# Kernel tuning notes

Hardware: AMD Instinct MI355X
Metric: run time of the kernel (lower is better)

The kernel has to match this reference:

```python
import jax, jax.numpy as jnp
import numpy as np
from jax import lax

DN = ('NCDHW', 'OIDHW', 'NCDHW')


def _ln(x, w, b, eps=1e-5):
    m = jnp.mean(x, -1, keepdims=True)
    v = jnp.mean((x - m) ** 2, -1, keepdims=True)
    return (x - m) * lax.rsqrt(v + eps) * w + b


def _gelu(x):
    return jax.nn.gelu(x, approximate=False)


def _dwconv3(v, w, b, groups):
    # depthwise 3x3x3, padding=1, stride=1; v:[B,C,H,W,D], w:[C,1,3,3,3]
    y = lax.conv_general_dilated(v, w, (1, 1, 1), 'SAME',
                                 dimension_numbers=DN,
                                 feature_group_count=groups)
    return y + b[None, :, None, None, None]


def _forward(x, ln1_w, ln1_b, q_w, sr1_w, sr1_b, n1_w, n1_b, sr2_w, sr2_b,
             n2_w, n2_b, kv1_w, kv2_w, lc1_w, lc1_b, lc2_w, lc2_b,
             proj_w, proj_b, ln2_w, ln2_b, fc1_w, fc1_b, fc2_w, fc2_b,
             H, W, D):
    B, N, C = x.shape
    h = 8
    h2 = h // 2
    hd = C // h
    scale = hd ** -0.5
    C2 = C // 2

    # ---- pre-norm + attention ----
    xa = _ln(x, ln1_w, ln1_b)
    q = (xa @ q_w.T).reshape(B, N, h, hd).transpose(0, 2, 1, 3)  # [B,h,N,hd]

    x_ = xa.transpose(0, 2, 1).reshape(B, C, H, W, D)
    # branch 1: conv k=2 s=2 spatial reduction
    y1 = lax.conv_general_dilated(x_, sr1_w, (2, 2, 2), 'VALID',
                                  dimension_numbers=DN) + sr1_b[None, :, None, None, None]
    N1 = (H // 2) * (W // 2) * (D // 2)
    x1 = _gelu(_ln(y1.reshape(B, C, N1).transpose(0, 2, 1), n1_w, n1_b))  # [B,N1,C]
    # branch 2: 1x1x1 conv, full resolution
    y2 = lax.conv_general_dilated(x_, sr2_w, (1, 1, 1), 'VALID',
                                  dimension_numbers=DN) + sr2_b[None, :, None, None, None]
    N2 = N
    x2 = _gelu(_ln(y2.reshape(B, C, N2).transpose(0, 2, 1), n2_w, n2_b))  # [B,N2,C]

    kv1 = (x1 @ kv1_w.T).reshape(B, N1, 2, h2, hd).transpose(2, 0, 3, 1, 4)
    k1, v1 = kv1[0], kv1[1]  # [B,h2,N1,hd]
    kv2 = (x2 @ kv2_w.T).reshape(B, N2, 2, h2, hd).transpose(2, 0, 3, 1, 4)
    k2, v2 = kv2[0], kv2[1]  # [B,h2,N2,hd]

    attn1 = jax.nn.softmax(jnp.einsum('bhnd,bhmd->bhnm', q[:, :h2], k1) * scale, axis=-1)
    v1sp = v1.transpose(0, 2, 1, 3).reshape(B, N1, C2).transpose(0, 2, 1).reshape(
        B, C2, H // 2, W // 2, D // 2)
    v1 = v1 + _dwconv3(v1sp, lc1_w, lc1_b, C2).reshape(B, h2, hd, N1).transpose(0, 1, 3, 2)
    o1 = jnp.einsum('bhnm,bhmd->bhnd', attn1, v1).transpose(0, 2, 1, 3).reshape(B, N, C2)

    attn2 = jax.nn.softmax(jnp.einsum('bhnd,bhmd->bhnm', q[:, h2:], k2) * scale, axis=-1)
    v2sp = v2.transpose(0, 2, 1, 3).reshape(B, N2, C2).transpose(0, 2, 1).reshape(B, C2, H, W, D)
    v2 = v2 + _dwconv3(v2sp, lc2_w, lc2_b, C2).reshape(B, h2, hd, N2).transpose(0, 1, 3, 2)
    o2 = jnp.einsum('bhnm,bhmd->bhnd', attn2, v2).transpose(0, 2, 1, 3).reshape(B, N, C2)

    att = jnp.concatenate([o1, o2], axis=-1) @ proj_w.T + proj_b
    x = x + att  # residual (drop_path = 0)

    # ---- pre-norm + MLP ----
    xm = _ln(x, ln2_w, ln2_b)
    mlp = _gelu(xm @ fc1_w.T + fc1_b) @ fc2_w.T + fc2_b
    return x + mlp


def setup_inputs() -> dict:
    key = jax.random.key(0)
    B, C, H, W, D = 2, 384, 16, 16, 16
    N = H * W * D
    hid = 4 * C
    C2 = C // 2
    ks = iter(jax.random.split(key, 32))
    rn = lambda shape, s=0.02: (jax.random.normal(next(ks), shape) * s).astype(jnp.float32)
    return {
        'x': jax.random.normal(next(ks), (B, N, C), jnp.float32),
        'ln1_w': jnp.ones(C, jnp.float32), 'ln1_b': jnp.zeros(C, jnp.float32),
        'q_w': rn((C, C)),
        'sr1_w': rn((C, C, 2, 2, 2), 0.025), 'sr1_b': jnp.zeros(C, jnp.float32),
        'n1_w': jnp.ones(C, jnp.float32), 'n1_b': jnp.zeros(C, jnp.float32),
        'sr2_w': rn((C, C, 1, 1, 1), 0.07), 'sr2_b': jnp.zeros(C, jnp.float32),
        'n2_w': jnp.ones(C, jnp.float32), 'n2_b': jnp.zeros(C, jnp.float32),
        'kv1_w': rn((C, C)), 'kv2_w': rn((C, C)),
        'lc1_w': rn((C2, 1, 3, 3, 3), 0.27), 'lc1_b': jnp.zeros(C2, jnp.float32),
        'lc2_w': rn((C2, 1, 3, 3, 3), 0.27), 'lc2_b': jnp.zeros(C2, jnp.float32),
        'proj_w': rn((C, C)), 'proj_b': jnp.zeros(C, jnp.float32),
        'ln2_w': jnp.ones(C, jnp.float32), 'ln2_b': jnp.zeros(C, jnp.float32),
        'fc1_w': rn((hid, C)), 'fc1_b': jnp.zeros(hid, jnp.float32),
        'fc2_w': rn((C, hid)), 'fc2_b': jnp.zeros(C, jnp.float32),
        'H': H, 'W': W, 'D': D,
    }


def reference(x, ln1_w, ln1_b, q_w, sr1_w, sr1_b, n1_w, n1_b, sr2_w, sr2_b,
              n2_w, n2_b, kv1_w, kv2_w, lc1_w, lc1_b, lc2_w, lc2_b,
              proj_w, proj_b, ln2_w, ln2_b, fc1_w, fc1_b, fc2_w, fc2_b,
              H, W, D):
    return _forward(x, ln1_w, ln1_b, q_w, sr1_w, sr1_b, n1_w, n1_b, sr2_w, sr2_b,
                    n2_w, n2_b, kv1_w, kv2_w, lc1_w, lc1_b, lc2_w, lc2_b,
                    proj_w, proj_b, ln2_w, ln2_b, fc1_w, fc1_b, fc2_w, fc2_b,
                    H, W, D)
```

## Files before the change

### kernel.cpp

```cpp
#include <hip/hip_runtime.h>

typedef unsigned short ushort_t;
typedef unsigned int uint_t;
typedef __bf16 bf16_t;
typedef __bf16 bf16x8 __attribute__((ext_vector_type(8)));
typedef float f32x4 __attribute__((ext_vector_type(4)));

__device__ __forceinline__ float b2f(ushort_t u) {
    union { uint_t i; float f; } v; v.i = ((uint_t)u) << 16; return v.f;
}
__device__ __forceinline__ ushort_t f2b(float f) {
    union { float f; uint_t i; } v; v.f = f;
    uint_t r = v.i + 0x7fffu + ((v.i >> 16) & 1u);
    return (ushort_t)(r >> 16);
}
__device__ __forceinline__ float gelu_exact(float x) {
    return 0.5f * x * (1.0f + erff(x * 0.70710678118654752f));
}

__global__ void prep_weights(const float* __restrict__ q_w, const float* __restrict__ sr2_w,
                             const float* __restrict__ kv1_w, const float* __restrict__ kv2_w,
                             const float* __restrict__ proj_w, const float* __restrict__ fc1_w,
                             const float* __restrict__ fc2_w, const float* __restrict__ sr1_w,
                             ushort_t* __restrict__ dst) {
    int gid = blockIdx.x * 256 + threadIdx.x;
    int i = gid;
    if (i < 147456) { dst[gid] = f2b(q_w[i]); return; }
    i -= 147456;
    if (i < 147456) { dst[gid] = f2b(sr2_w[i]); return; }
    i -= 147456;
    if (i < 147456) { dst[gid] = f2b(kv1_w[i]); return; }
    i -= 147456;
    if (i < 147456) { dst[gid] = f2b(kv2_w[i]); return; }
    i -= 147456;
    if (i < 147456) { dst[gid] = f2b(proj_w[i]); return; }
    i -= 147456;
    if (i < 589824) { dst[gid] = f2b(fc1_w[i]); return; }
    i -= 589824;
    if (i < 589824) { dst[gid] = f2b(fc2_w[i]); return; }
    i -= 589824;
    if (i < 1179648) {
        int co = i / 3072, r = i % 3072, kk = r / 384, ci = r % 384;
        dst[gid] = f2b(sr1_w[((size_t)co * 384 + ci) * 8 + kk]);
    }
}

__global__ void im2col_kernel(const ushort_t* __restrict__ xa, ushort_t* __restrict__ A1) {
    int gid = blockIdx.x * 256 + threadIdx.x;
    if (gid >= 1024 * 3072) return;
    int m = gid / 3072, r = gid % 3072, kk = r / 384, ci = r % 384;
    int b = m >> 9, n1 = m & 511;
    int ho = n1 >> 6, wo = (n1 >> 3) & 7, dz = n1 & 7;
    int n = ((2 * ho + ((kk >> 2) & 1)) << 8) + ((2 * wo + ((kk >> 1) & 1)) << 4) + (2 * dz + (kk & 1));
    A1[gid] = xa[((size_t)b * 4096 + n) * 384 + ci];
}

__global__ __launch_bounds__(128) void ln_kernel(const float* __restrict__ in,
                                                 const float* __restrict__ w,
                                                 const float* __restrict__ b,
                                                 float* __restrict__ outf,
                                                 ushort_t* __restrict__ outb, int act) {
    const int C = 384;
    int row = blockIdx.x, tid = threadIdx.x;
    size_t base = (size_t)row * C;
    float x[3], s = 0.f, s2 = 0.f;
#pragma unroll
    for (int i = 0; i < 3; i++) {
        int c = tid + i * 128;
        float v = in[base + c];
        x[i] = v; s += v; s2 += v * v;
    }
    for (int off = 32; off; off >>= 1) { s += __shfl_down(s, off); s2 += __shfl_down(s2, off); }
    __shared__ float sc[4];
    int lane = tid & 63, wid = tid >> 6;
    if (lane == 0) { sc[wid] = s; sc[wid + 2] = s2; }
    __syncthreads();
    float ts = sc[0] + sc[1], ts2 = sc[2] + sc[3];
    float mean = ts / C;
    float var = ts2 / C - mean * mean;
    float rstd = rsqrtf(var + 1e-5f);
#pragma unroll
    for (int i = 0; i < 3; i++) {
        int c = tid + i * 128;
        float v = (x[i] - mean) * rstd * w[c] + b[c];
        if (act) v = gelu_exact(v);
        if (outf) outf[base + c] = v;
        if (outb) outb[base + c] = f2b(v);
    }
}

__global__ __launch_bounds__(256) void mfma_gemm(const ushort_t* __restrict__ A,
                                                 const ushort_t* __restrict__ W,
                                                 const float* __restrict__ bias,
                                                 const float* __restrict__ res,
                                                 float* __restrict__ outf,
                                                 ushort_t* __restrict__ outb,
                                                 int M, int N, int K, int act) {
    __shared__ bf16_t Asl[128][40];
    __shared__ bf16_t Wsl[128][40];
    int tid = threadIdx.x;
    int wave = tid >> 6, lane = tid & 63, g = lane >> 4, c = lane & 15;
    int wm = wave >> 1, wn = wave & 1;
    int m0 = blockIdx.y * 128, n0 = blockIdx.x * 128;
    int srow = tid >> 1, sseg = tid & 1;

    f32x4 acc[4][4];
#pragma unroll
    for (int i = 0; i < 4; i++)
#pragma unroll
        for (int j = 0; j < 4; j++) acc[i][j] = f32x4{0.f, 0.f, 0.f, 0.f};

    for (int k0 = 0; k0 < K; k0 += 32) {
        const ushort_t* As = A + (size_t)(m0 + srow) * K + k0 + sseg * 16;
        const ushort_t* Ws = W + (size_t)(n0 + srow) * K + k0 + sseg * 16;
        uint4 av0 = *(const uint4*)As, av1 = *(const uint4*)(As + 8);
        uint4 wv0 = *(const uint4*)Ws, wv1 = *(const uint4*)(Ws + 8);
        __syncthreads();
        *(uint4*)&Asl[srow][sseg * 16] = av0;
        *(uint4*)&Asl[srow][sseg * 16 + 8] = av1;
        *(uint4*)&Wsl[srow][sseg * 16] = wv0;
        *(uint4*)&Wsl[srow][sseg * 16 + 8] = wv1;
        __syncthreads();
        bf16x8 af[4], bf[4];
#pragma unroll
        for (int fi = 0; fi < 4; fi++) af[fi] = *(bf16x8*)&Asl[wm * 64 + fi * 16 + c][g * 8];
#pragma unroll
        for (int fj = 0; fj < 4; fj++) bf[fj] = *(bf16x8*)&Wsl[wn * 64 + fj * 16 + c][g * 8];
#pragma unroll
        for (int fi = 0; fi < 4; fi++)
#pragma unroll
            for (int fj = 0; fj < 4; fj++)
                acc[fi][fj] = __builtin_amdgcn_mfma_f32_16x16x32_bf16(af[fi], bf[fj], acc[fi][fj], 0, 0, 0);
    }

#pragma unroll
    for (int fi = 0; fi < 4; fi++) {
#pragma unroll
        for (int fj = 0; fj < 4; fj++) {
            int n = n0 + wn * 64 + fj * 16 + c;
            float bv = bias ? bias[n] : 0.f;
#pragma unroll
            for (int i = 0; i < 4; i++) {
                int m = m0 + wm * 64 + fi * 16 + 4 * g + i;
                float v = acc[fi][fj][i] + bv;
                if (act == 1) v = gelu_exact(v);
                size_t idx = (size_t)m * N + n;
                if (res) v += res[idx];
                if (outf) outf[idx] = v;
                if (outb) outb[idx] = f2b(v);
            }
        }
    }
}

__global__ __launch_bounds__(256) void gemm64(const ushort_t* __restrict__ A,
                                              const ushort_t* __restrict__ W,
                                              const float* __restrict__ bias,
                                              const float* __restrict__ res,
                                              float* __restrict__ outf,
                                              ushort_t* __restrict__ outb,
                                              int M, int N, int K, int act, float oscale) {
    __shared__ bf16_t Asl[64][72];
    __shared__ bf16_t Wsl[64][72];
    int tid = threadIdx.x;
    int wave = tid >> 6, lane = tid & 63, g = lane >> 4, c = lane & 15;
    int wm = wave >> 1, wn = wave & 1;
    int m0 = blockIdx.y * 64, n0 = blockIdx.x * 64;
    int srow = tid >> 2, sseg = tid & 3;

    f32x4 acc[2][2];
#pragma unroll
    for (int i = 0; i < 2; i++)
#pragma unroll
        for (int j = 0; j < 2; j++) acc[i][j] = f32x4{0.f, 0.f, 0.f, 0.f};

    for (int k0 = 0; k0 < K; k0 += 64) {
        const ushort_t* As = A + (size_t)(m0 + srow) * K + k0 + sseg * 16;
        const ushort_t* Ws = W + (size_t)(n0 + srow) * K + k0 + sseg * 16;
        uint4 av0 = *(const uint4*)As, av1 = *(const uint4*)(As + 8);
        uint4 wv0 = *(const uint4*)Ws, wv1 = *(const uint4*)(Ws + 8);
        __syncthreads();
        *(uint4*)&Asl[srow][sseg * 16] = av0;
        *(uint4*)&Asl[srow][sseg * 16 + 8] = av1;
        *(uint4*)&Wsl[srow][sseg * 16] = wv0;
        *(uint4*)&Wsl[srow][sseg * 16 + 8] = wv1;
        __syncthreads();
#pragma unroll
        for (int kk = 0; kk < 2; kk++) {
            bf16x8 af[2], bf[2];
#pragma unroll
            for (int fi = 0; fi < 2; fi++) af[fi] = *(bf16x8*)&Asl[wm * 32 + fi * 16 + c][kk * 32 + g * 8];
#pragma unroll
            for (int fj = 0; fj < 2; fj++) bf[fj] = *(bf16x8*)&Wsl[wn * 32 + fj * 16 + c][kk * 32 + g * 8];
#pragma unroll
            for (int fi = 0; fi < 2; fi++)
#pragma unroll
                for (int fj = 0; fj < 2; fj++)
                    acc[fi][fj] = __builtin_amdgcn_mfma_f32_16x16x32_bf16(af[fi], bf[fj], acc[fi][fj], 0, 0, 0);
        }
    }

#pragma unroll
    for (int fi = 0; fi < 2; fi++) {
#pragma unroll
        for (int fj = 0; fj < 2; fj++) {
            int n = n0 + wn * 32 + fj * 16 + c;
            float bv = bias ? bias[n] : 0.f;
#pragma unroll
            for (int i = 0; i < 4; i++) {
                int m = m0 + wm * 32 + fi * 16 + 4 * g + i;
                float v = (acc[fi][fj][i] + bv) * oscale;
                if (act == 1) v = gelu_exact(v);
                size_t idx = (size_t)m * N + n;
                if (res) v += res[idx];
                if (outf) outf[idx] = v;
                if (outb) outb[idx] = f2b(v);
            }
        }
    }
}

__global__ void dwconv_kernel(const ushort_t* __restrict__ vin,
                              const float* __restrict__ wt,
                              const float* __restrict__ bias,
                              ushort_t* __restrict__ vout,
                              int Hs, int Wsz, int Ds, int S, int total) {
    int gid = blockIdx.x * 256 + threadIdx.x;
    if (gid >= total) return;
    int c2 = gid % 192;
    int r = gid / 192;
    int n = r % S;
    int b = r / S;
    int dz = n % Ds, wy = (n / Ds) % Wsz, hx = n / (Wsz * Ds);
    float center = b2f(vin[(size_t)(b * S + n) * 384 + c2]);
    float acc = bias[c2];
    for (int kh = -1; kh <= 1; kh++) {
        int h2 = hx + kh; if (h2 < 0 || h2 >= Hs) continue;
        for (int kw = -1; kw <= 1; kw++) {
            int w2 = wy + kw; if (w2 < 0 || w2 >= Wsz) continue;
            for (int kd = -1; kd <= 1; kd++) {
                int d2 = dz + kd; if (d2 < 0 || d2 >= Ds) continue;
                int nn = (h2 * Wsz + w2) * Ds + d2;
                acc += b2f(vin[(size_t)(b * S + nn) * 384 + c2]) *
                       wt[c2 * 27 + (kh + 1) * 9 + (kw + 1) * 3 + (kd + 1)];
            }
        }
    }
    vout[(size_t)(b * S + n) * 192 + c2] = f2b(center + acc);
}

__global__ __launch_bounds__(256) void transpose_kernel(const ushort_t* __restrict__ src,
                                                        ushort_t* __restrict__ dst, int S) {
    __shared__ ushort_t t_lds[64][65];
    int n0 = blockIdx.x * 64, c0 = blockIdx.y * 64, b = blockIdx.z;
    int tid = threadIdx.x;
#pragma unroll
    for (int i = 0; i < 16; i++) {
        int idx = tid + i * 256;
        int r = idx >> 6, cc = idx & 63;
        t_lds[r][cc] = src[((size_t)b * S + n0 + r) * 192 + c0 + cc];
    }
    __syncthreads();
#pragma unroll
    for (int i = 0; i < 16; i++) {
        int idx = tid + i * 256;
        int r = idx >> 6, cc = idx & 63;
        dst[((size_t)b * 192 + c0 + r) * S + n0 + cc] = t_lds[cc][r];
    }
}

__global__ __launch_bounds__(256, 4) void attn_mfma5(
    const ushort_t* __restrict__ qbuf,
    const ushort_t* __restrict__ kv1,
    const ushort_t* __restrict__ kv2,
    const ushort_t* __restrict__ vt1,
    const ushort_t* __restrict__ vt2,
    ushort_t* __restrict__ obuf)
{
    __shared__ __align__(16) char lds_raw[18432];
    bf16_t (*P)[32][72] = (bf16_t (*)[32][72])lds_raw;
    float (*CF)[64][14] = (float (*)[64][14])lds_raw;

    const int N = 4096;
    int tid = threadIdx.x;
    int q0 = blockIdx.x * 32, hl = 7 - blockIdx.y, b = blockIdx.z;
    int wave = tid >> 6, lane = tid & 63, g = lane >> 4, c = lane & 15;
    int br2 = hl >> 2;
    int NK = br2 ? 4096 : 512;
    const ushort_t* kbuf = br2 ? kv2 : kv1;
    const ushort_t* vtb  = br2 ? vt2 : vt1;
    int hloc = hl & 3;
    int NKc = NK >> 2;
    int kb0 = wave * NKc;
    int nkt = NKc >> 6;

    union { uint4 u; bf16x8 v; } zz; zz.u = uint4{0u, 0u, 0u, 0u};
    const bf16x8 zero8 = zz.v;

    bf16x8 bq0[2], bq1[2];
#pragma unroll
    for (int qg = 0; qg < 2; qg++) {
        const ushort_t* qrowp = qbuf + ((size_t)b * N + q0 + qg * 16 + c) * 384 + hl * 48;
        bq0[qg] = *(const bf16x8*)(qrowp + g * 8);
        bq1[qg] = (g < 2) ? *(const bf16x8*)(qrowp + 32 + g * 8) : zero8;
    }

    f32x4 of[3][2];
#pragma unroll
    for (int dt = 0; dt < 3; dt++)
#pragma unroll
        for (int qg = 0; qg < 2; qg++) of[dt][qg] = f32x4{0.f, 0.f, 0.f, 0.f};
    float l_acc[2] = {0.f, 0.f};

    const ushort_t* kp = kbuf + ((size_t)b * NK + kb0 + c) * 384 + hloc * 48;
    const ushort_t* vp = vtb + ((size_t)b * 192 + hloc * 48 + c) * NK + kb0;

    for (int kt = 0; kt < nkt; kt++) {
        f32x4 sf[4][2];
#pragma unroll
        for (int t = 0; t < 4; t++)
#pragma unroll
            for (int qg = 0; qg < 2; qg++) sf[t][qg] = f32x4{0.f, 0.f, 0.f, 0.f};
#pragma unroll
        for (int t = 0; t < 4; t++) {
            const ushort_t* kr = kp + (size_t)(kt * 64 + 16 * t) * 384;
            bf16x8 ak0 = *(const bf16x8*)(kr + g * 8);
            bf16x8 ak1 = (g < 2) ? *(const bf16x8*)(kr + 32 + g * 8) : zero8;
#pragma unroll
            for (int qg = 0; qg < 2; qg++) {
                sf[t][qg] = __builtin_amdgcn_mfma_f32_16x16x32_bf16(ak0, bq0[qg], sf[t][qg], 0, 0, 0);
                sf[t][qg] = __builtin_amdgcn_mfma_f32_16x16x32_bf16(ak1, bq1[qg], sf[t][qg], 0, 0, 0);
            }
        }

#pragma unroll
        for (int qg = 0; qg < 2; qg++) {
#pragma unroll
            for (int t = 0; t < 4; t++) {
                union { ushort4 v; bf16_t h[4]; } pk;
#pragma unroll
                for (int i = 0; i < 4; i++) {
                    float p = exp2f(sf[t][qg][i]);
                    l_acc[qg] += p;
                    pk.h[i] = (bf16_t)p;
                }
                *(ushort4*)&P[wave][qg * 16 + c][16 * t + 4 * g] = pk.v;
            }
        }

        asm volatile("s_waitcnt lgkmcnt(0)" ::: "memory");

        bf16x8 pb0[2], pb1[2];
#pragma unroll
        for (int qg = 0; qg < 2; qg++) {
            pb0[qg] = *(bf16x8*)&P[wave][qg * 16 + c][g * 8];
            pb1[qg] = *(bf16x8*)&P[wave][qg * 16 + c][32 + g * 8];
        }
#pragma unroll
        for (int dt = 0; dt < 3; dt++) {
            const ushort_t* vr = vp + (size_t)(16 * dt) * NK + kt * 64;
            bf16x8 av0 = *(const bf16x8*)(vr + g * 8);
            bf16x8 av1 = *(const bf16x8*)(vr + 32 + g * 8);
#pragma unroll
            for (int qg = 0; qg < 2; qg++) {
                of[dt][qg] = __builtin_amdgcn_mfma_f32_16x16x32_bf16(av0, pb0[qg], of[dt][qg], 0, 0, 0);
                of[dt][qg] = __builtin_amdgcn_mfma_f32_16x16x32_bf16(av1, pb1[qg], of[dt][qg], 0, 0, 0);
            }
        }
    }

#pragma unroll
    for (int qg = 0; qg < 2; qg++) {
        l_acc[qg] += __shfl_xor(l_acc[qg], 16);
        l_acc[qg] += __shfl_xor(l_acc[qg], 32);
    }

#pragma unroll
    for (int qg = 0; qg < 2; qg++) {
        __syncthreads();
        float* cfp = &CF[wave][lane][0];
#pragma unroll
        for (int dt = 0; dt < 3; dt++)
#pragma unroll
            for (int i = 0; i < 4; i++) cfp[dt * 4 + i] = of[dt][qg][i];
        cfp[12] = l_acc[qg];
        __syncthreads();
        if (wave == 0) {
            float lsum = 0.f;
            float oc[12];
#pragma unroll
            for (int j = 0; j < 12; j++) oc[j] = 0.f;
#pragma unroll
            for (int w = 0; w < 4; w++) {
                lsum += CF[w][lane][12];
#pragma unroll
                for (int j = 0; j < 12; j++) oc[j] += CF[w][lane][j];
            }
            float rl = 1.f / lsum;
            int qrow = q0 + qg * 16 + c;
#pragma unroll
            for (int dt = 0; dt < 3; dt++) {
                union { ushort4 v; bf16_t h[4]; } pk;
#pragma unroll
                for (int i = 0; i < 4; i++) pk.h[i] = (bf16_t)(oc[dt * 4 + i] * rl);
                *(ushort4*)&obuf[((size_t)b * N + qrow) * 384 + hl * 48 + 16 * dt + 4 * g] = pk.v;
            }
        }
    }
}

extern "C" void kernel_launch(void* const* d_in, const int* in_sizes, int n_in,
                              void* d_out, int out_size, void* d_ws, size_t ws_size,
                              hipStream_t stream) {
    const int B = 2, N = 4096, C = 384, N1 = 512, HID = 1536;
    const float* x      = (const float*)d_in[0];
    const float* ln1_w  = (const float*)d_in[1];
    const float* ln1_b  = (const float*)d_in[2];
    const float* q_w    = (const float*)d_in[3];
    const float* sr1_w  = (const float*)d_in[4];
    const float* sr1_b  = (const float*)d_in[5];
    const float* n1_w   = (const float*)d_in[6];
    const float* n1_b   = (const float*)d_in[7];
    const float* sr2_w  = (const float*)d_in[8];
    const float* sr2_b  = (const float*)d_in[9];
    const float* n2_w   = (const float*)d_in[10];
    const float* n2_b   = (const float*)d_in[11];
    const float* kv1_w  = (const float*)d_in[12];
    const float* kv2_w  = (const float*)d_in[13];
    const float* lc1_w  = (const float*)d_in[14];
    const float* lc1_b  = (const float*)d_in[15];
    const float* lc2_w  = (const float*)d_in[16];
    const float* lc2_b  = (const float*)d_in[17];
    const float* proj_w = (const float*)d_in[18];
    const float* proj_b = (const float*)d_in[19];
    const float* ln2_w  = (const float*)d_in[20];
    const float* ln2_b  = (const float*)d_in[21];
    const float* fc1_w  = (const float*)d_in[22];
    const float* fc1_b  = (const float*)d_in[23];
    const float* fc2_w  = (const float*)d_in[24];
    const float* fc2_b  = (const float*)d_in[25];
    float* out = (float*)d_out;

    char* ws = (char*)d_ws;
    ushort_t* wbase = (ushort_t*)ws;
    ushort_t* wq   = wbase;
    ushort_t* wsr2 = wbase + 147456;
    ushort_t* wkv1 = wbase + 294912;
    ushort_t* wkv2 = wbase + 442368;
    ushort_t* wproj= wbase + 589824;
    ushort_t* wfc1 = wbase + 737280;
    ushort_t* wfc2 = wbase + 1327104;
    ushort_t* wsr1 = wbase + 1916928;
    ushort_t* xa_bf = (ushort_t*)(ws + 6193152);
    ushort_t* qbB   = (ushort_t*)(ws + 12484608);
    ushort_t* x2_bf = (ushort_t*)(ws + 18776064);
    ushort_t* kv2   = (ushort_t*)(ws + 25067520);
    ushort_t* vmod2 = (ushort_t*)(ws + 31358976);
    ushort_t* kv1   = (ushort_t*)(ws + 34504704);
    ushort_t* vmod1 = (ushort_t*)(ws + 35291136);
    ushort_t* x1_bf = (ushort_t*)(ws + 35684352);
    float*    y2f   = (float*)(ws + 36470784);
    float*    y1f   = (float*)(ws + 49053696);
    ushort_t* A1    = (ushort_t*)(ws + 50626560);
    ushort_t* hid   = (ushort_t*)(ws + 56918016);
    ushort_t* vt2   = (ushort_t*)(ws + 82083840);
    ushort_t* vt1   = (ushort_t*)(ws + 85229568);
    ushort_t* Obuf  = xa_bf;
    float*    xres  = y2f;
    ushort_t* xm_bf = A1;

    const float QSCALE = 0.14433756729740643f * 1.4426950408889634f;

    prep_weights<<<(3096576 + 255) / 256, 256, 0, stream>>>(q_w, sr2_w, kv1_w, kv2_w,
                                                            proj_w, fc1_w, fc2_w, sr1_w, wbase);
    ln_kernel<<<B * N, 128, 0, stream>>>(x, ln1_w, ln1_b, nullptr, xa_bf, 0);
    gemm64<<<dim3(6, 128), 256, 0, stream>>>(xa_bf, wq, nullptr, nullptr,
                                             nullptr, qbB, B * N, C, C, 0, QSCALE);
    gemm64<<<dim3(6, 128), 256, 0, stream>>>(xa_bf, wsr2, sr2_b, nullptr,
                                             y2f, nullptr, B * N, C, C, 0, 1.f);
    ln_kernel<<<B * N, 128, 0, stream>>>(y2f, n2_w, n2_b, nullptr, x2_bf, 1);
    im2col_kernel<<<(1024 * 3072 + 255) / 256, 256, 0, stream>>>(xa_bf, A1);
    gemm64<<<dim3(6, 16), 256, 0, stream>>>(A1, wsr1, sr1_b, nullptr,
                                            y1f, nullptr, 1024, C, 3072, 0, 1.f);
    ln_kernel<<<B * N1, 128, 0, stream>>>(y1f, n1_w, n1_b, nullptr, x1_bf, 1);
    gemm64<<<dim3(6, 128), 256, 0, stream>>>(x2_bf, wkv2, nullptr, nullptr,
                                             nullptr, kv2, B * N, C, C, 0, 1.f);
    gemm64<<<dim3(6, 16), 256, 0, stream>>>(x1_bf, wkv1, nullptr, nullptr,
                                            nullptr, kv1, 1024, C, C, 0, 1.f);
    {
        int total2 = B * N * 192;
        dwconv_kernel<<<(total2 + 255) / 256, 256, 0, stream>>>(kv2 + 192, lc2_w, lc2_b, vmod2,
                                                                16, 16, 16, N, total2);
        int total1 = B * N1 * 192;
        dwconv_kernel<<<(total1 + 255) / 256, 256, 0, stream>>>(kv1 + 192, lc1_w, lc1_b, vmod1,
                                                                8, 8, 8, N1, total1);
        transpose_kernel<<<dim3(64, 3, 2), 256, 0, stream>>>(vmod2, vt2, 4096);
        transpose_kernel<<<dim3(8, 3, 2), 256, 0, stream>>>(vmod1, vt1, 512);
    }
    attn_mfma5<<<dim3(N / 32, 8, B), 256, 0, stream>>>(qbB, kv1, kv2, vt1, vt2, Obuf);
    gemm64<<<dim3(6, 128), 256, 0, stream>>>(Obuf, wproj, proj_b, x,
                                             xres, nullptr, B * N, C, C, 0, 1.f);
    ln_kernel<<<B * N, 128, 0, stream>>>(xres, ln2_w, ln2_b, nullptr, xm_bf, 0);
    mfma_gemm<<<dim3(12, 64), 256, 0, stream>>>(xm_bf, wfc1, fc1_b, nullptr,
                                                nullptr, hid, B * N, HID, C, 1);
    gemm64<<<dim3(6, 128), 256, 0, stream>>>(hid, wfc2, fc2_b, xres,
                                             out, nullptr, B * N, C, HID, 0, 1.f);
}
```

Measured before the change: 350.9 us.

## Double-buffer K/V register loads in attention and fuse q/sr2 GEMMs

The attention kernel now prefetches the next K tile and the current V tile into registers before computing each tile. It unrolls the loop by two with ping-pong K buffers and raises MFMA priority with s_setprio, so global load latency overlaps with compute. Occupancy is lowered from 4 to 3 blocks per CU to leave room for the extra registers. Separately, the q projection and the sr2 1x1 conv GEMMs, which read the same input, are merged into one launch over the concatenated weight, saving a launch and a second pass over xa. The unroll by two assumes an even number of key tiles, and the K1 load no longer zeroes lanes with g>=2, relying on the zero bq1 entries to cancel them.

```diff
diff --git a/kernel.cpp b/kernel.cpp
--- a/kernel.cpp
+++ b/kernel.cpp
@@ -215,6 +215,73 @@
                 if (res) v += res[idx];
                 if (outf) outf[idx] = v;
                 if (outb) outb[idx] = f2b(v);
+            }
+        }
+    }
+}
+
+__global__ __launch_bounds__(256) void gemm_qy2(const ushort_t* __restrict__ A,
+                                                const ushort_t* __restrict__ W,
+                                                const float* __restrict__ sr2_b,
+                                                ushort_t* __restrict__ qb,
+                                                float* __restrict__ y2f,
+                                                int M, float qscale) {
+    const int K = 384;
+    __shared__ bf16_t Asl[64][72];
+    __shared__ bf16_t Wsl[64][72];
+    int tid = threadIdx.x;
+    int wave = tid >> 6, lane = tid & 63, g = lane >> 4, c = lane & 15;
+    int wm = wave >> 1, wn = wave & 1;
+    int m0 = blockIdx.y * 64, n0 = blockIdx.x * 64;
+    int srow = tid >> 2, sseg = tid & 3;
+
+    f32x4 acc[2][2];
+#pragma unroll
+    for (int i = 0; i < 2; i++)
+#pragma unroll
+        for (int j = 0; j < 2; j++) acc[i][j] = f32x4{0.f, 0.f, 0.f, 0.f};
+
+    for (int k0 = 0; k0 < K; k0 += 64) {
+        const ushort_t* As = A + (size_t)(m0 + srow) * K + k0 + sseg * 16;
+        const ushort_t* Ws = W + (size_t)(n0 + srow) * K + k0 + sseg * 16;
+        uint4 av0 = *(const uint4*)As, av1 = *(const uint4*)(As + 8);
+        uint4 wv0 = *(const uint4*)Ws, wv1 = *(const uint4*)(Ws + 8);
+        __syncthreads();
+        *(uint4*)&Asl[srow][sseg * 16] = av0;
+        *(uint4*)&Asl[srow][sseg * 16 + 8] = av1;
+        *(uint4*)&Wsl[srow][sseg * 16] = wv0;
+        *(uint4*)&Wsl[srow][sseg * 16 + 8] = wv1;
+        __syncthreads();
+#pragma unroll
+        for (int kk = 0; kk < 2; kk++) {
+            bf16x8 af[2], bf[2];
+#pragma unroll
+            for (int fi = 0; fi < 2; fi++) af[fi] = *(bf16x8*)&Asl[wm * 32 + fi * 16 + c][kk * 32 + g * 8];
+#pragma unroll
+            for (int fj = 0; fj < 2; fj++) bf[fj] = *(bf16x8*)&Wsl[wn * 32 + fj * 16 + c][kk * 32 + g * 8];
+#pragma unroll
+            for (int fi = 0; fi < 2; fi++)
+#pragma unroll
+                for (int fj = 0; fj < 2; fj++)
+                    acc[fi][fj] = __builtin_amdgcn_mfma_f32_16x16x32_bf16(af[fi], bf[fj], acc[fi][fj], 0, 0, 0);
+        }
+    }
+
+    int isq = (n0 < 384);
+#pragma unroll
+    for (int fi = 0; fi < 2; fi++) {
+#pragma unroll
+        for (int fj = 0; fj < 2; fj++) {
+            int n = n0 + wn * 32 + fj * 16 + c;
+#pragma unroll
+            for (int i = 0; i < 4; i++) {
+                int m = m0 + wm * 32 + fi * 16 + 4 * g + i;
+                float v = acc[fi][fj][i];
+                if (isq) {
+                    qb[(size_t)m * 384 + n] = f2b(v * qscale);
+                } else {
+                    y2f[(size_t)m * 384 + (n - 384)] = v + sr2_b[n - 384];
+                }
             }
         }
     }
@@ -269,7 +336,7 @@
     }
 }
 
-__global__ __launch_bounds__(256, 4) void attn_mfma5(
+__global__ __launch_bounds__(256, 3) void attn_mfma6(
     const ushort_t* __restrict__ qbuf,
     const ushort_t* __restrict__ kv1,
     const ushort_t* __restrict__ kv2,
@@ -315,59 +382,89 @@
     const ushort_t* kp = kbuf + ((size_t)b * NK + kb0 + c) * 384 + hloc * 48;
     const ushort_t* vp = vtb + ((size_t)b * 192 + hloc * 48 + c) * NK + kb0;
 
-    for (int kt = 0; kt < nkt; kt++) {
-        f32x4 sf[4][2];
-#pragma unroll
-        for (int t = 0; t < 4; t++)
-#pragma unroll
-            for (int qg = 0; qg < 2; qg++) sf[t][qg] = f32x4{0.f, 0.f, 0.f, 0.f};
-#pragma unroll
-        for (int t = 0; t < 4; t++) {
-            const ushort_t* kr = kp + (size_t)(kt * 64 + 16 * t) * 384;
-            bf16x8 ak0 = *(const bf16x8*)(kr + g * 8);
-            bf16x8 ak1 = (g < 2) ? *(const bf16x8*)(kr + 32 + g * 8) : zero8;
-#pragma unroll
-            for (int qg = 0; qg < 2; qg++) {
-                sf[t][qg] = __builtin_amdgcn_mfma_f32_16x16x32_bf16(ak0, bq0[qg], sf[t][qg], 0, 0, 0);
-                sf[t][qg] = __builtin_amdgcn_mfma_f32_16x16x32_bf16(ak1, bq1[qg], sf[t][qg], 0, 0, 0);
-            }
-        }
-
-#pragma unroll
-        for (int qg = 0; qg < 2; qg++) {
-#pragma unroll
-            for (int t = 0; t < 4; t++) {
-                union { ushort4 v; bf16_t h[4]; } pk;
-#pragma unroll
-                for (int i = 0; i < 4; i++) {
-                    float p = exp2f(sf[t][qg][i]);
-                    l_acc[qg] += p;
-                    pk.h[i] = (bf16_t)p;
-                }
-                *(ushort4*)&P[wave][qg * 16 + c][16 * t + 4 * g] = pk.v;
-            }
-        }
-
-        asm volatile("s_waitcnt lgkmcnt(0)" ::: "memory");
-
-        bf16x8 pb0[2], pb1[2];
-#pragma unroll
-        for (int qg = 0; qg < 2; qg++) {
-            pb0[qg] = *(bf16x8*)&P[wave][qg * 16 + c][g * 8];
-            pb1[qg] = *(bf16x8*)&P[wave][qg * 16 + c][32 + g * 8];
-        }
-#pragma unroll
-        for (int dt = 0; dt < 3; dt++) {
-            const ushort_t* vr = vp + (size_t)(16 * dt) * NK + kt * 64;
-            bf16x8 av0 = *(const bf16x8*)(vr + g * 8);
-            bf16x8 av1 = *(const bf16x8*)(vr + 32 + g * 8);
-#pragma unroll
-            for (int qg = 0; qg < 2; qg++) {
-                of[dt][qg] = __builtin_amdgcn_mfma_f32_16x16x32_bf16(av0, pb0[qg], of[dt][qg], 0, 0, 0);
-                of[dt][qg] = __builtin_amdgcn_mfma_f32_16x16x32_bf16(av1, pb1[qg], of[dt][qg], 0, 0, 0);
-            }
-        }
-    }
+    bf16x8 kA0[4], kA1[4], kB0[4], kB1[4];
+    bf16x8 av0[3], av1[3];
+
+#define LOAD_K(d0, d1, kt_) do {                                               \
+    const ushort_t* kr_ = kp + (size_t)((kt_) * 64) * 384;                     \
+    _Pragma("unroll")                                                          \
+    for (int t_ = 0; t_ < 4; t_++) {                                           \
+        d0[t_] = *(const bf16x8*)(kr_ + (size_t)(16 * t_) * 384 + g * 8);      \
+        d1[t_] = *(const bf16x8*)(kr_ + (size_t)(16 * t_) * 384 + 32 + g * 8); \
+    } } while (0)
+
+#define LOAD_V(kt_) do {                                                       \
+    const ushort_t* vr_ = vp + (kt_) * 64;                                     \
+    _Pragma("unroll")                                                          \
+    for (int dt_ = 0; dt_ < 3; dt_++) {                                        \
+        av0[dt_] = *(const bf16x8*)(vr_ + (size_t)(16 * dt_) * NK + g * 8);    \
+        av1[dt_] = *(const bf16x8*)(vr_ + (size_t)(16 * dt_) * NK + 32 + g * 8); \
+    } } while (0)
+
+#define ATTN_TILE(K0, K1) do {                                                 \
+    f32x4 sf[4][2];                                                            \
+    _Pragma("unroll")                                                          \
+    for (int t_ = 0; t_ < 4; t_++)                                             \
+        _Pragma("unroll")                                                      \
+        for (int qg_ = 0; qg_ < 2; qg_++) sf[t_][qg_] = f32x4{0.f, 0.f, 0.f, 0.f}; \
+    __builtin_amdgcn_s_setprio(1);                                             \
+    _Pragma("unroll")                                                          \
+    for (int t_ = 0; t_ < 4; t_++) {                                           \
+        _Pragma("unroll")                                                      \
+        for (int qg_ = 0; qg_ < 2; qg_++) {                                    \
+            sf[t_][qg_] = __builtin_amdgcn_mfma_f32_16x16x32_bf16(K0[t_], bq0[qg_], sf[t_][qg_], 0, 0, 0); \
+            sf[t_][qg_] = __builtin_amdgcn_mfma_f32_16x16x32_bf16(K1[t_], bq1[qg_], sf[t_][qg_], 0, 0, 0); \
+        }                                                                      \
+    }                                                                          \
+    __builtin_amdgcn_s_setprio(0);                                             \
+    _Pragma("unroll")                                                          \
+    for (int qg_ = 0; qg_ < 2; qg_++) {                                        \
+        _Pragma("unroll")                                                      \
+        for (int t_ = 0; t_ < 4; t_++) {                                       \
+            union { ushort4 v; bf16_t h[4]; } pk_;                             \
+            _Pragma("unroll")                                                  \
+            for (int i_ = 0; i_ < 4; i_++) {                                   \
+                float p_ = exp2f(sf[t_][qg_][i_]);                             \
+                l_acc[qg_] += p_;                                              \
+                pk_.h[i_] = (bf16_t)p_;                                        \
+            }                                                                  \
+            *(ushort4*)&P[wave][qg_ * 16 + c][16 * t_ + 4 * g] = pk_.v;        \
+        }                                                                      \
+    }                                                                          \
+    asm volatile("s_waitcnt lgkmcnt(0)" ::: "memory");                         \
+    {                                                                          \
+        bf16x8 pb0_[2], pb1_[2];                                               \
+        _Pragma("unroll")                                                      \
+        for (int qg_ = 0; qg_ < 2; qg_++) {                                    \
+            pb0_[qg_] = *(bf16x8*)&P[wave][qg_ * 16 + c][g * 8];               \
+            pb1_[qg_] = *(bf16x8*)&P[wave][qg_ * 16 + c][32 + g * 8];          \
+        }                                                                      \
+        __builtin_amdgcn_s_setprio(1);                                         \
+        _Pragma("unroll")                                                      \
+        for (int dt_ = 0; dt_ < 3; dt_++) {                                    \
+            _Pragma("unroll")                                                  \
+            for (int qg_ = 0; qg_ < 2; qg_++) {                                \
+                of[dt_][qg_] = __builtin_amdgcn_mfma_f32_16x16x32_bf16(av0[dt_], pb0_[qg_], of[dt_][qg_], 0, 0, 0); \
+                of[dt_][qg_] = __builtin_amdgcn_mfma_f32_16x16x32_bf16(av1[dt_], pb1_[qg_], of[dt_][qg_], 0, 0, 0); \
+            }                                                                  \
+        }                                                                      \
+        __builtin_amdgcn_s_setprio(0);                                         \
+    } } while (0)
+
+    LOAD_K(kA0, kA1, 0);
+    for (int kt = 0; kt < nkt; kt += 2) {
+        LOAD_V(kt);
+        LOAD_K(kB0, kB1, kt + 1);
+        asm volatile("" ::: "memory");
+        ATTN_TILE(kA0, kA1);
+        LOAD_V(kt + 1);
+        if (kt + 2 < nkt) LOAD_K(kA0, kA1, kt + 2);
+        asm volatile("" ::: "memory");
+        ATTN_TILE(kB0, kB1);
+    }
+#undef LOAD_K
+#undef LOAD_V
+#undef ATTN_TILE
 
 #pragma unroll
     for (int qg = 0; qg < 2; qg++) {
@@ -443,8 +540,7 @@
 
     char* ws = (char*)d_ws;
     ushort_t* wbase = (ushort_t*)ws;
-    ushort_t* wq   = wbase;
-    ushort_t* wsr2 = wbase + 147456;
+    ushort_t* wqy2 = wbase;
     ushort_t* wkv1 = wbase + 294912;
     ushort_t* wkv2 = wbase + 442368;
     ushort_t* wproj= wbase + 589824;
@@ -474,10 +570,7 @@
     prep_weights<<<(3096576 + 255) / 256, 256, 0, stream>>>(q_w, sr2_w, kv1_w, kv2_w,
                                                             proj_w, fc1_w, fc2_w, sr1_w, wbase);
     ln_kernel<<<B * N, 128, 0, stream>>>(x, ln1_w, ln1_b, nullptr, xa_bf, 0);
-    gemm64<<<dim3(6, 128), 256, 0, stream>>>(xa_bf, wq, nullptr, nullptr,
-                                             nullptr, qbB, B * N, C, C, 0, QSCALE);
-    gemm64<<<dim3(6, 128), 256, 0, stream>>>(xa_bf, wsr2, sr2_b, nullptr,
-                                             y2f, nullptr, B * N, C, C, 0, 1.f);
+    gemm_qy2<<<dim3(12, 128), 256, 0, stream>>>(xa_bf, wqy2, sr2_b, qbB, y2f, B * N, QSCALE);
     ln_kernel<<<B * N, 128, 0, stream>>>(y2f, n2_w, n2_b, nullptr, x2_bf, 1);
     im2col_kernel<<<(1024 * 3072 + 255) / 256, 256, 0, stream>>>(xa_bf, A1);
     gemm64<<<dim3(6, 16), 256, 0, stream>>>(A1, wsr1, sr1_b, nullptr,
@@ -497,7 +590,7 @@
         transpose_kernel<<<dim3(64, 3, 2), 256, 0, stream>>>(vmod2, vt2, 4096);
         transpose_kernel<<<dim3(8, 3, 2), 256, 0, stream>>>(vmod1, vt1, 512);
     }
-    attn_mfma5<<<dim3(N / 32, 8, B), 256, 0, stream>>>(qbB, kv1, kv2, vt1, vt2, Obuf);
+    attn_mfma6<<<dim3(N / 32, 8, B), 256, 0, stream>>>(qbB, kv1, kv2, vt1, vt2, Obuf);
     gemm64<<<dim3(6, 128), 256, 0, stream>>>(Obuf, wproj, proj_b, x,
                                              xres, nullptr, B * N, C, C, 0, 1.f);
     ln_kernel<<<B * N, 128, 0, stream>>>(xres, ln2_w, ln2_b, nullptr, xm_bf, 0);
```

Measured after the change: 420.1 us. 19.7% more time.
